# Kernel optimization log

Measured on AMD Instinct MI355X. Metric: run time of the kernel, lower is better.

## Reference

```python
import jax, jax.numpy as jnp
import numpy as np

N, E, G = 2048, 4096, 16
IN_DIM, HID, E_DIM, EDGE_H = 11, 128, 6, 64
EPS = 1e-5


def setup_inputs() -> dict:
    key = jax.random.key(0)
    ks = jax.random.split(key, 32)
    s = 0.1  # keep activations tame
    inp = {
        "h": jax.random.normal(ks[0], (N, IN_DIM), jnp.float32),
        "e": jax.random.normal(ks[1], (E, E_DIM), jnp.float32),
        "src": jax.random.randint(ks[2], (E,), 0, N, jnp.int32),
        "dst": jax.random.randint(ks[3], (E,), 0, N, jnp.int32),
        "node_graph": (jnp.arange(N, dtype=jnp.int32) // (N // G)),
        # layer 0 (in_dim=11 -> hid=128)
        "eW1_0": jax.random.normal(ks[4], (E_DIM, EDGE_H), jnp.float32) * s,
        "eb1_0": jax.random.normal(ks[5], (EDGE_H,), jnp.float32) * s,
        "eW2_0": jax.random.normal(ks[6], (EDGE_H, IN_DIM * HID), jnp.float32) * s,
        "eb2_0": jax.random.normal(ks[7], (IN_DIM * HID,), jnp.float32) * s,
        "bias_0": jax.random.normal(ks[8], (HID,), jnp.float32) * s,
        "gamma_0": jax.random.uniform(ks[9], (HID,), jnp.float32, 0.5, 1.5),
        "beta_0": jax.random.normal(ks[10], (HID,), jnp.float32) * s,
        "mean_0": jax.random.normal(ks[11], (HID,), jnp.float32) * s,
        "var_0": jax.random.uniform(ks[12], (HID,), jnp.float32, 0.5, 1.5),
        # layers 1..3 stacked (hid -> hid)
        "eW1": jax.random.normal(ks[13], (3, E_DIM, EDGE_H), jnp.float32) * s,
        "eb1": jax.random.normal(ks[14], (3, EDGE_H), jnp.float32) * s,
        "eW2": jax.random.normal(ks[15], (3, EDGE_H, HID * HID), jnp.float32) * s,
        "eb2": jax.random.normal(ks[16], (3, HID * HID), jnp.float32) * s,
        "bias": jax.random.normal(ks[17], (3, HID), jnp.float32) * s,
        "gamma": jax.random.uniform(ks[18], (3, HID), jnp.float32, 0.5, 1.5),
        "beta": jax.random.normal(ks[19], (3, HID), jnp.float32) * s,
        "mean": jax.random.normal(ks[20], (3, HID), jnp.float32) * s,
        "var": jax.random.uniform(ks[21], (3, HID), jnp.float32, 0.5, 1.5),
        # output BN (on mean readout)
        "g_out": jax.random.uniform(ks[22], (HID,), jnp.float32, 0.5, 1.5),
        "b_out": jax.random.normal(ks[23], (HID,), jnp.float32) * s,
        "m_out": jax.random.normal(ks[24], (HID,), jnp.float32) * s,
        "v_out": jax.random.uniform(ks[25], (HID,), jnp.float32, 0.5, 1.5),
    }
    return inp


def _bn(x, ga, be, mu, vv):
    return (x - mu) * jax.lax.rsqrt(vv + EPS) * ga + be


def _nn_layer(x, e, src, dst, W1, b1, W2, b2, bb, ga, be, mu, vv, din):
    # edge MLP -> per-edge weight matrix [E, din, HID]
    w = (jax.nn.relu(e @ W1 + b1) @ W2 + b2).reshape(E, din, HID)
    msg = jnp.einsum('ei,eio->eo', x[src], w)          # per-edge message [E, HID]
    agg = jax.ops.segment_sum(msg, dst, num_segments=N)
    deg = jax.ops.segment_sum(jnp.ones((E,), x.dtype), dst, num_segments=N)
    agg = agg / jnp.maximum(deg, 1.0)[:, None] + bb    # mean aggregation + NNConv bias
    return _bn(jax.nn.relu(agg), ga, be, mu, vv)       # relu -> BatchNorm (eval)


def reference(h, e, src, dst, node_graph, eW1_0, eb1_0, eW2_0, eb2_0, bias_0,
              gamma_0, beta_0, mean_0, var_0, eW1, eb1, eW2, eb2, bias,
              gamma, beta, mean, var, g_out, b_out, m_out, v_out):
    x = _nn_layer(h, e, src, dst, eW1_0, eb1_0, eW2_0, eb2_0, bias_0,
                  gamma_0, beta_0, mean_0, var_0, IN_DIM)
    for i in range(3):
        x = _nn_layer(x, e, src, dst, eW1[i], eb1[i], eW2[i], eb2[i], bias[i],
                      gamma[i], beta[i], mean[i], var[i], HID)
    # dropout is identity in eval mode
    cnt = jax.ops.segment_sum(jnp.ones((N,), x.dtype), node_graph, num_segments=G)
    hn = jax.ops.segment_sum(x, node_graph, num_segments=G) / cnt[:, None]
    hx = jax.ops.segment_max(x, node_graph, num_segments=G)
    hn = _bn(hn, g_out, b_out, m_out, v_out)
    return jnp.concatenate([hn, hx], axis=1)  # [G, 2*HID]
```

## Files before the change

### kernel.cpp

```cpp
#include <hip/hip_runtime.h>
#include <stdint.h>

#define N_NODES 2048
#define N_EDGES 4096
#define N_GRAPH 16
#define IN_DIM  11
#define HID     128
#define E_DIMF  6
#define EDGE_H  64
#define NSLICE  65
#define ZCOLS   (NSLICE*HID)
#define BN_EPS  1e-5f

typedef __attribute__((ext_vector_type(8))) short short8;
typedef __attribute__((ext_vector_type(4))) float f32x4;

static __device__ __forceinline__ float bf2f(unsigned short u) {
  union { float f; uint32_t i; } x; x.i = ((uint32_t)u) << 16; return x.f;
}
static __device__ __forceinline__ unsigned short f2bf(float f) {
  union { float f; uint32_t i; } x; x.f = f;
  uint32_t i = x.i;
  return (unsigned short)((i + 0x7FFFu + ((i >> 16) & 1u)) >> 16);
}

__global__ void calc_deg_i(const int* __restrict__ dst, int* __restrict__ degi) {
  int e = blockIdx.x * 256 + threadIdx.x;
  if (e < N_EDGES) atomicAdd(&degi[dst[e]], 1);
}

__global__ __launch_bounds__(256) void build_offsets(const int* __restrict__ degi,
                                                     int* __restrict__ roff,
                                                     int* __restrict__ cursor) {
  __shared__ int part[256];
  int t = threadIdx.x;
  int base = t * 8;
  int loc[8];
  int s = 0;
#pragma unroll
  for (int j = 0; j < 8; ++j) { loc[j] = s; s += degi[base + j]; }
  part[t] = s;
  __syncthreads();
  int pre = 0;
  for (int i = 0; i < t; ++i) pre += part[i];
#pragma unroll
  for (int j = 0; j < 8; ++j) {
    int v = pre + loc[j];
    roff[base + j] = v;
    cursor[base + j] = v;
  }
  if (t == 255) roff[N_NODES] = pre + s;
}

__global__ void scatter_edges(const int* __restrict__ dst, int* __restrict__ cursor,
                              int* __restrict__ elist) {
  int e = blockIdx.x * 256 + threadIdx.x;
  if (e < N_EDGES) {
    int pos = atomicAdd(&cursor[dst[e]], 1);
    elist[pos] = e;
  }
}

__global__ __launch_bounds__(256) void conv_w0(const float* __restrict__ W2,
                                               const float* __restrict__ b2,
                                               unsigned short* __restrict__ WbT) {
  __shared__ unsigned short tile[128 * 130];
  const int k = blockIdx.x;
  const float* src = (k < 64) ? (W2 + (size_t)k * IN_DIM * HID) : b2;
  const int t = threadIdx.x;
  for (int j = t; j < IN_DIM * HID; j += 256) {
    int i = j >> 7, o = j & 127;
    tile[i * 130 + o] = f2bf(src[j]);
  }
  __syncthreads();
  for (int j = t; j < HID * 32; j += 256) {
    int o = j >> 5, i = j & 31;
    unsigned short v = (i < IN_DIM) ? tile[i * 130 + o] : (unsigned short)0;
    WbT[((size_t)k * HID + o) * 32 + i] = v;
  }
}

__global__ __launch_bounds__(256) void conv_wL(const float* __restrict__ W2,
                                               const float* __restrict__ b2,
                                               unsigned short* __restrict__ WbT) {
  __shared__ unsigned short tile[128 * 130];
  const int k = blockIdx.x, l = blockIdx.y;
  const float* src = (k < 64) ? (W2 + ((size_t)l * 64 + k) * (HID * HID))
                              : (b2 + (size_t)l * (HID * HID));
  unsigned short* dstp = WbT + (size_t)l * ZCOLS * HID;
  const int t = threadIdx.x;
  for (int j = t; j < HID * HID; j += 256) {
    int i = j >> 7, o = j & 127;
    tile[i * 130 + o] = f2bf(src[j]);
  }
  __syncthreads();
  for (int j = t; j < HID * HID; j += 256) {
    int o = j >> 7, i = j & 127;
    dstp[((size_t)k * HID + o) * HID + i] = tile[i * 130 + o];
  }
}

__global__ void conv_x0(const float* __restrict__ h, unsigned short* __restrict__ xb0) {
  int idx = blockIdx.x * 256 + threadIdx.x;
  if (idx >= N_NODES * 32) return;
  int n = idx >> 5, i = idx & 31;
  xb0[idx] = f2bf(i < IN_DIM ? h[n * IN_DIM + i] : 0.0f);
}

template <int KP, int SWZ>
__global__ __launch_bounds__(256) void gemm_z(const unsigned short* __restrict__ Xb,
                                              const unsigned short* __restrict__ WbT,
                                              unsigned short* __restrict__ Z) {
  extern __shared__ unsigned short lds[];
  unsigned short* Al = lds;
  unsigned short* Bl = lds + 128 * KP;
  const int nb = blockIdx.x;
  const int mb = blockIdx.y;
  const int t = threadIdx.x;
  const int ROWB = KP * 2;
  const int NCH = 128 * ROWB / 16;
  const unsigned short* Asrc = Xb + (size_t)mb * 128 * KP;
  const unsigned short* Bsrc = WbT + (size_t)nb * 128 * KP;
  for (int c = t; c < NCH; c += 256) {
    int off = c * 16;
    int row = off / ROWB;
    int kb = off % ROWB;
    int dsto = row * ROWB + (kb ^ ((row & SWZ) << 4));
    *(uint4*)((char*)Al + dsto) = *(const uint4*)((const char*)Asrc + off);
    *(uint4*)((char*)Bl + dsto) = *(const uint4*)((const char*)Bsrc + off);
  }
  __syncthreads();

  const int w = t >> 6, l = t & 63;
  const int wm = (w >> 1) * 64, wn = (w & 1) * 64;
  const int lr = l & 15, lh = l >> 4;
  f32x4 acc[4][4] = {};
#pragma unroll
  for (int kk = 0; kk < KP; kk += 32) {
    short8 a[4], b[4];
    const int kb = (kk + lh * 8) * 2;
#pragma unroll
    for (int mi = 0; mi < 4; ++mi) {
      int row = wm + mi * 16 + lr;
      int addr = row * ROWB + (kb ^ ((row & SWZ) << 4));
      a[mi] = *(const short8*)((const char*)Al + addr);
    }
#pragma unroll
    for (int ni = 0; ni < 4; ++ni) {
      int col = wn + ni * 16 + lr;
      int addr = col * ROWB + (kb ^ ((col & SWZ) << 4));
      b[ni] = *(const short8*)((const char*)Bl + addr);
    }
#pragma unroll
    for (int mi = 0; mi < 4; ++mi)
#pragma unroll
      for (int ni = 0; ni < 4; ++ni)
        acc[mi][ni] = __builtin_amdgcn_mfma_f32_16x16x32_bf16(a[mi], b[ni], acc[mi][ni], 0, 0, 0);
  }
#pragma unroll
  for (int mi = 0; mi < 4; ++mi) {
#pragma unroll
    for (int ni = 0; ni < 4; ++ni) {
#pragma unroll
      for (int r = 0; r < 4; ++r) {
        int grow = mb * 128 + wm + mi * 16 + lh * 4 + r;
        int gcol = nb * 128 + wn + ni * 16 + lr;
        Z[(size_t)grow * ZCOLS + gcol] = f2bf(acc[mi][ni][r]);
      }
    }
  }
}

template <int LAST>
__global__ __launch_bounds__(128) void node_gather(
    const float* __restrict__ efeat, const float* __restrict__ W1,
    const float* __restrict__ b1, const unsigned short* __restrict__ Z,
    const int* __restrict__ elist, const int* __restrict__ roff,
    const int* __restrict__ src,
    const float* __restrict__ bias, const float* __restrict__ gamma,
    const float* __restrict__ beta, const float* __restrict__ mean,
    const float* __restrict__ var,
    unsigned short* __restrict__ xbout,
    const int* __restrict__ ng, float* __restrict__ gsum,
    unsigned int* __restrict__ gmax, float* __restrict__ gcnt) {
  const int n = blockIdx.x, t = threadIdx.x;
  const int start = roff[n], end = roff[n + 1];
  __shared__ float hs[NSLICE + 1];
  float a0 = 0.f, a1 = 0.f, a2 = 0.f, a3 = 0.f;
  for (int idx = start; idx < end; ++idx) {
    const int e = elist[idx];
    if (t < EDGE_H) {
      float a = b1[t];
#pragma unroll
      for (int j = 0; j < E_DIMF; ++j) a += efeat[e * E_DIMF + j] * W1[j * EDGE_H + t];
      hs[t] = fmaxf(a, 0.f);
    } else if (t == EDGE_H) {
      hs[EDGE_H] = 1.f;
    }
    __syncthreads();
    const unsigned short* zr = Z + (size_t)src[e] * ZCOLS;
#pragma unroll 4
    for (int k = 0; k < 64; k += 4) {
      a0 += hs[k + 0] * bf2f(zr[(k + 0) * HID + t]);
      a1 += hs[k + 1] * bf2f(zr[(k + 1) * HID + t]);
      a2 += hs[k + 2] * bf2f(zr[(k + 2) * HID + t]);
      a3 += hs[k + 3] * bf2f(zr[(k + 3) * HID + t]);
    }
    a0 += bf2f(zr[64 * HID + t]);
    __syncthreads();
  }
  const int dg = end - start;
  float v = (a0 + a1 + a2 + a3) / (float)(dg > 0 ? dg : 1) + bias[t];
  v = fmaxf(v, 0.f);
  v = (v - mean[t]) * rsqrtf(var[t] + BN_EPS) * gamma[t] + beta[t];
  if (!LAST) {
    xbout[n * HID + t] = f2bf(v);
  } else {
    const int g = ng[n];
    atomicAdd(&gsum[g * HID + t], v);
    unsigned int u = __float_as_uint(v);
    unsigned int key = (u & 0x80000000u) ? ~u : (u | 0x80000000u);
    atomicMax(&gmax[g * HID + t], key);
    if (t == 0) atomicAdd(&gcnt[g], 1.f);
  }
}

__global__ void out_final(const float* __restrict__ gsum, const unsigned int* __restrict__ gmax,
                          const float* __restrict__ gcnt,
                          const float* __restrict__ g_out, const float* __restrict__ b_out,
                          const float* __restrict__ m_out, const float* __restrict__ v_out,
                          float* __restrict__ out) {
  int g = blockIdx.x, t = threadIdx.x;
  float hn = gsum[g * HID + t] / fmaxf(gcnt[g], 1.0f);
  hn = (hn - m_out[t]) * rsqrtf(v_out[t] + BN_EPS) * g_out[t] + b_out[t];
  unsigned int key = gmax[g * HID + t];
  unsigned int u = (key & 0x80000000u) ? (key ^ 0x80000000u) : ~key;
  out[g * 2 * HID + t] = hn;
  out[g * 2 * HID + HID + t] = __uint_as_float(u);
}

extern "C" void kernel_launch(void* const* d_in, const int* in_sizes, int n_in,
                              void* d_out, int out_size, void* d_ws, size_t ws_size,
                              hipStream_t stream) {
  const float* h_in   = (const float*)d_in[0];
  const float* e_in   = (const float*)d_in[1];
  const int*   src    = (const int*)d_in[2];
  const int*   dst    = (const int*)d_in[3];
  const int*   ng     = (const int*)d_in[4];
  const float* eW1_0  = (const float*)d_in[5];
  const float* eb1_0  = (const float*)d_in[6];
  const float* eW2_0  = (const float*)d_in[7];
  const float* eb2_0  = (const float*)d_in[8];
  const float* bias_0 = (const float*)d_in[9];
  const float* gamma_0= (const float*)d_in[10];
  const float* beta_0 = (const float*)d_in[11];
  const float* mean_0 = (const float*)d_in[12];
  const float* var_0  = (const float*)d_in[13];
  const float* eW1    = (const float*)d_in[14];
  const float* eb1    = (const float*)d_in[15];
  const float* eW2    = (const float*)d_in[16];
  const float* eb2    = (const float*)d_in[17];
  const float* biasL  = (const float*)d_in[18];
  const float* gammaL = (const float*)d_in[19];
  const float* betaL  = (const float*)d_in[20];
  const float* meanL  = (const float*)d_in[21];
  const float* varL   = (const float*)d_in[22];
  const float* g_out  = (const float*)d_in[23];
  const float* b_out  = (const float*)d_in[24];
  const float* m_out  = (const float*)d_in[25];
  const float* v_out  = (const float*)d_in[26];
  float* out = (float*)d_out;

  char* ws = (char*)d_ws;
  size_t off = 0;
  auto alloc = [&](size_t bytes) {
    void* p = ws + off;
    off = (off + bytes + 255) & ~(size_t)255;
    return p;
  };
  unsigned short* Z    = (unsigned short*)alloc((size_t)N_NODES * ZCOLS * 2);
  unsigned short* WbT0 = (unsigned short*)alloc((size_t)ZCOLS * 32 * 2);
  unsigned short* WbTL = (unsigned short*)alloc((size_t)3 * ZCOLS * HID * 2);
  unsigned short* xb0  = (unsigned short*)alloc((size_t)N_NODES * 32 * 2);
  unsigned short* xb   = (unsigned short*)alloc((size_t)N_NODES * HID * 2);
  float* gsum          = (float*)alloc((size_t)N_GRAPH * HID * 4);
  unsigned int* gmax   = (unsigned int*)alloc((size_t)N_GRAPH * HID * 4);
  float* gcnt          = (float*)alloc((size_t)N_GRAPH * 4);
  int*   degi          = (int*)alloc((size_t)N_NODES * 4);
  size_t zbytes = (size_t)((char*)(degi + N_NODES) - (char*)gsum);
  int* roff            = (int*)alloc((size_t)(N_NODES + 1) * 4);
  int* cursor          = (int*)alloc((size_t)N_NODES * 4);
  int* elist           = (int*)alloc((size_t)N_EDGES * 4);

  hipMemsetAsync(gsum, 0, zbytes, stream);
  calc_deg_i<<<N_EDGES / 256, 256, 0, stream>>>(dst, degi);
  build_offsets<<<1, 256, 0, stream>>>(degi, roff, cursor);
  scatter_edges<<<N_EDGES / 256, 256, 0, stream>>>(dst, cursor, elist);
  conv_w0<<<65, 256, 0, stream>>>(eW2_0, eb2_0, WbT0);
  conv_wL<<<dim3(65, 3), 256, 0, stream>>>(eW2, eb2, WbTL);
  conv_x0<<<(N_NODES * 32) / 256, 256, 0, stream>>>(h_in, xb0);

  gemm_z<32, 3><<<dim3(65, 16), 256, 2 * 128 * 32 * 2, stream>>>(xb0, WbT0, Z);
  node_gather<0><<<N_NODES, 128, 0, stream>>>(e_in, eW1_0, eb1_0, Z, elist, roff, src,
                                              bias_0, gamma_0, beta_0, mean_0, var_0,
                                              xb, ng, gsum, gmax, gcnt);

  for (int l = 0; l < 3; ++l) {
    gemm_z<128, 7><<<dim3(65, 16), 256, 2 * 128 * 128 * 2, stream>>>(
        xb, WbTL + (size_t)l * ZCOLS * HID, Z);
    if (l < 2) {
      node_gather<0><<<N_NODES, 128, 0, stream>>>(
          e_in, eW1 + l * E_DIMF * EDGE_H, eb1 + l * EDGE_H, Z, elist, roff, src,
          biasL + l * HID, gammaL + l * HID, betaL + l * HID, meanL + l * HID,
          varL + l * HID, xb, ng, gsum, gmax, gcnt);
    } else {
      node_gather<1><<<N_NODES, 128, 0, stream>>>(
          e_in, eW1 + l * E_DIMF * EDGE_H, eb1 + l * EDGE_H, Z, elist, roff, src,
          biasL + l * HID, gammaL + l * HID, betaL + l * HID, meanL + l * HID,
          varL + l * HID, xb, ng, gsum, gmax, gcnt);
    }
  }

  out_final<<<N_GRAPH, HID, 0, stream>>>(gsum, gmax, gcnt, g_out, b_out, m_out, v_out, out);
}
```

Before: 202.5 us.

## Vectorize Z stores and gather loads, merge prep kernels into one launch

Merges the three weight/input conversion kernels into a single prep launch, which removes launch overhead. The MFMA operands are swapped so each lane holds four consecutive output columns, letting Z be written as packed ushort4 stores instead of scalar 2-byte stores. node_gather now has each thread load 8 bf16 values at once across a k-slice and then reduces the partial sums through shared memory. This trades extra LDS traffic and a barrier for wider, coalesced global loads.

```diff
diff --git a/kernel.cpp b/kernel.cpp
--- a/kernel.cpp
+++ b/kernel.cpp
@@ -61,50 +61,51 @@
   }
 }
 
-__global__ __launch_bounds__(256) void conv_w0(const float* __restrict__ W2,
-                                               const float* __restrict__ b2,
-                                               unsigned short* __restrict__ WbT) {
+__global__ __launch_bounds__(256) void prep(const float* __restrict__ W2_0,
+                                            const float* __restrict__ b2_0,
+                                            const float* __restrict__ W2L,
+                                            const float* __restrict__ b2L,
+                                            const float* __restrict__ h_in,
+                                            unsigned short* __restrict__ WbT0,
+                                            unsigned short* __restrict__ WbTL,
+                                            unsigned short* __restrict__ xb0) {
+  const int y = blockIdx.y, t = threadIdx.x;
+  if (y == 4) {
+    for (int idx = blockIdx.x * 256 + t; idx < N_NODES * 32; idx += 65 * 256) {
+      int n = idx >> 5, i = idx & 31;
+      xb0[idx] = f2bf(i < IN_DIM ? h_in[n * IN_DIM + i] : 0.0f);
+    }
+    return;
+  }
   __shared__ unsigned short tile[128 * 130];
   const int k = blockIdx.x;
-  const float* src = (k < 64) ? (W2 + (size_t)k * IN_DIM * HID) : b2;
-  const int t = threadIdx.x;
-  for (int j = t; j < IN_DIM * HID; j += 256) {
-    int i = j >> 7, o = j & 127;
-    tile[i * 130 + o] = f2bf(src[j]);
-  }
-  __syncthreads();
-  for (int j = t; j < HID * 32; j += 256) {
-    int o = j >> 5, i = j & 31;
-    unsigned short v = (i < IN_DIM) ? tile[i * 130 + o] : (unsigned short)0;
-    WbT[((size_t)k * HID + o) * 32 + i] = v;
-  }
-}
-
-__global__ __launch_bounds__(256) void conv_wL(const float* __restrict__ W2,
-                                               const float* __restrict__ b2,
-                                               unsigned short* __restrict__ WbT) {
-  __shared__ unsigned short tile[128 * 130];
-  const int k = blockIdx.x, l = blockIdx.y;
-  const float* src = (k < 64) ? (W2 + ((size_t)l * 64 + k) * (HID * HID))
-                              : (b2 + (size_t)l * (HID * HID));
-  unsigned short* dstp = WbT + (size_t)l * ZCOLS * HID;
-  const int t = threadIdx.x;
-  for (int j = t; j < HID * HID; j += 256) {
-    int i = j >> 7, o = j & 127;
-    tile[i * 130 + o] = f2bf(src[j]);
-  }
-  __syncthreads();
-  for (int j = t; j < HID * HID; j += 256) {
-    int o = j >> 7, i = j & 127;
-    dstp[((size_t)k * HID + o) * HID + i] = tile[i * 130 + o];
-  }
-}
-
-__global__ void conv_x0(const float* __restrict__ h, unsigned short* __restrict__ xb0) {
-  int idx = blockIdx.x * 256 + threadIdx.x;
-  if (idx >= N_NODES * 32) return;
-  int n = idx >> 5, i = idx & 31;
-  xb0[idx] = f2bf(i < IN_DIM ? h[n * IN_DIM + i] : 0.0f);
+  if (y == 0) {
+    const float* src = (k < 64) ? (W2_0 + (size_t)k * IN_DIM * HID) : b2_0;
+    for (int j = t; j < IN_DIM * HID; j += 256) {
+      int i = j >> 7, o = j & 127;
+      tile[i * 130 + o] = f2bf(src[j]);
+    }
+    __syncthreads();
+    for (int j = t; j < HID * 32; j += 256) {
+      int o = j >> 5, i = j & 31;
+      WbT0[((size_t)k * HID + o) * 32 + i] =
+          (i < IN_DIM) ? tile[i * 130 + o] : (unsigned short)0;
+    }
+  } else {
+    const int l = y - 1;
+    const float* src = (k < 64) ? (W2L + ((size_t)l * 64 + k) * (HID * HID))
+                                : (b2L + (size_t)l * (HID * HID));
+    unsigned short* dstp = WbTL + (size_t)l * ZCOLS * HID;
+    for (int j = t; j < HID * HID; j += 256) {
+      int i = j >> 7, o = j & 127;
+      tile[i * 130 + o] = f2bf(src[j]);
+    }
+    __syncthreads();
+    for (int j = t; j < HID * HID; j += 256) {
+      int o = j >> 7, i = j & 127;
+      dstp[((size_t)k * HID + o) * HID + i] = tile[i * 130 + o];
+    }
+  }
 }
 
 template <int KP, int SWZ>
@@ -155,18 +156,20 @@
     for (int mi = 0; mi < 4; ++mi)
 #pragma unroll
       for (int ni = 0; ni < 4; ++ni)
-        acc[mi][ni] = __builtin_amdgcn_mfma_f32_16x16x32_bf16(a[mi], b[ni], acc[mi][ni], 0, 0, 0);
+        acc[mi][ni] = __builtin_amdgcn_mfma_f32_16x16x32_bf16(b[ni], a[mi], acc[mi][ni], 0, 0, 0);
   }
 #pragma unroll
   for (int mi = 0; mi < 4; ++mi) {
+    const int node = mb * 128 + wm + mi * 16 + lr;
+    unsigned short* zp = Z + (size_t)node * ZCOLS + nb * 128 + wn + lh * 4;
 #pragma unroll
     for (int ni = 0; ni < 4; ++ni) {
-#pragma unroll
-      for (int r = 0; r < 4; ++r) {
-        int grow = mb * 128 + wm + mi * 16 + lh * 4 + r;
-        int gcol = nb * 128 + wn + ni * 16 + lr;
-        Z[(size_t)grow * ZCOLS + gcol] = f2bf(acc[mi][ni][r]);
-      }
+      ushort4 pk;
+      pk.x = f2bf(acc[mi][ni][0]);
+      pk.y = f2bf(acc[mi][ni][1]);
+      pk.z = f2bf(acc[mi][ni][2]);
+      pk.w = f2bf(acc[mi][ni][3]);
+      *(ushort4*)(zp + ni * 16) = pk;
     }
   }
 }
@@ -184,44 +187,56 @@
     const int* __restrict__ ng, float* __restrict__ gsum,
     unsigned int* __restrict__ gmax, float* __restrict__ gcnt) {
   const int n = blockIdx.x, t = threadIdx.x;
+  const int cg = t & 15, kg = t >> 4;
   const int start = roff[n], end = roff[n + 1];
-  __shared__ float hs[NSLICE + 1];
-  float a0 = 0.f, a1 = 0.f, a2 = 0.f, a3 = 0.f;
+  __shared__ float hs[EDGE_H];
+  __shared__ float red[128][9];
+  float acc8[8] = {};
   for (int idx = start; idx < end; ++idx) {
     const int e = elist[idx];
+    __syncthreads();
     if (t < EDGE_H) {
       float a = b1[t];
 #pragma unroll
       for (int j = 0; j < E_DIMF; ++j) a += efeat[e * E_DIMF + j] * W1[j * EDGE_H + t];
       hs[t] = fmaxf(a, 0.f);
-    } else if (t == EDGE_H) {
-      hs[EDGE_H] = 1.f;
     }
     __syncthreads();
-    const unsigned short* zr = Z + (size_t)src[e] * ZCOLS;
-#pragma unroll 4
-    for (int k = 0; k < 64; k += 4) {
-      a0 += hs[k + 0] * bf2f(zr[(k + 0) * HID + t]);
-      a1 += hs[k + 1] * bf2f(zr[(k + 1) * HID + t]);
-      a2 += hs[k + 2] * bf2f(zr[(k + 2) * HID + t]);
-      a3 += hs[k + 3] * bf2f(zr[(k + 3) * HID + t]);
-    }
-    a0 += bf2f(zr[64 * HID + t]);
-    __syncthreads();
-  }
+    const unsigned short* zr = Z + (size_t)src[e] * ZCOLS + cg * 8;
+#pragma unroll
+    for (int kk = 0; kk < 8; ++kk) {
+      const int k = kg * 8 + kk;
+      short8 v = *(const short8*)(zr + k * HID);
+      const float hk = hs[k];
+#pragma unroll
+      for (int j = 0; j < 8; ++j) acc8[j] += hk * bf2f((unsigned short)v[j]);
+    }
+    if (kg == 0) {
+      short8 v = *(const short8*)(zr + 64 * HID);
+#pragma unroll
+      for (int j = 0; j < 8; ++j) acc8[j] += bf2f((unsigned short)v[j]);
+    }
+  }
+#pragma unroll
+  for (int j = 0; j < 8; ++j) red[t][j] = acc8[j];
+  __syncthreads();
+  const int o = t;
+  float s = 0.f;
+#pragma unroll
+  for (int k2 = 0; k2 < 8; ++k2) s += red[k2 * 16 + (o >> 3)][o & 7];
   const int dg = end - start;
-  float v = (a0 + a1 + a2 + a3) / (float)(dg > 0 ? dg : 1) + bias[t];
+  float v = s / (float)(dg > 0 ? dg : 1) + bias[o];
   v = fmaxf(v, 0.f);
-  v = (v - mean[t]) * rsqrtf(var[t] + BN_EPS) * gamma[t] + beta[t];
+  v = (v - mean[o]) * rsqrtf(var[o] + BN_EPS) * gamma[o] + beta[o];
   if (!LAST) {
-    xbout[n * HID + t] = f2bf(v);
+    xbout[n * HID + o] = f2bf(v);
   } else {
     const int g = ng[n];
-    atomicAdd(&gsum[g * HID + t], v);
+    atomicAdd(&gsum[g * HID + o], v);
     unsigned int u = __float_as_uint(v);
     unsigned int key = (u & 0x80000000u) ? ~u : (u | 0x80000000u);
-    atomicMax(&gmax[g * HID + t], key);
-    if (t == 0) atomicAdd(&gcnt[g], 1.f);
+    atomicMax(&gmax[g * HID + o], key);
+    if (o == 0) atomicAdd(&gcnt[g], 1.f);
   }
 }
 
@@ -296,9 +311,7 @@
   calc_deg_i<<<N_EDGES / 256, 256, 0, stream>>>(dst, degi);
   build_offsets<<<1, 256, 0, stream>>>(degi, roff, cursor);
   scatter_edges<<<N_EDGES / 256, 256, 0, stream>>>(dst, cursor, elist);
-  conv_w0<<<65, 256, 0, stream>>>(eW2_0, eb2_0, WbT0);
-  conv_wL<<<dim3(65, 3), 256, 0, stream>>>(eW2, eb2, WbTL);
-  conv_x0<<<(N_NODES * 32) / 256, 256, 0, stream>>>(h_in, xb0);
+  prep<<<dim3(65, 5), 256, 0, stream>>>(eW2_0, eb2_0, eW2, eb2, h_in, WbT0, WbTL, xb0);
 
   gemm_z<32, 3><<<dim3(65, 16), 256, 2 * 128 * 32 * 2, stream>>>(xb0, WbT0, Z);
   node_gather<0><<<N_NODES, 128, 0, stream>>>(e_in, eW1_0, eb1_0, Z, elist, roff, src,
```

Result: no change. 203.0 us (+0.2%).
